# Performance work log

Hardware: AMD Instinct MI355X
Metric: run time of the kernel (lower is better)

Reference implementation:

```python
import jax, jax.numpy as jnp
import numpy as np

B, N, C = 8, 16384, 40
E, KD, VD = 512, 256, 256


def setup_inputs() -> dict:
    key = jax.random.key(0)
    ks = jax.random.split(key, 10)
    s = 0.02
    return {
        "q": jax.random.normal(ks[0], (B, N, E), jnp.float32),
        "k": jax.random.normal(ks[1], (B, C, KD), jnp.float32),
        "v": jax.random.normal(ks[2], (B, C, VD), jnp.float32),
        "coarse_pred": jax.random.normal(ks[3], (B, C, N), jnp.float32),
        "Wq": jax.random.normal(ks[4], (E, E), jnp.float32) * s,
        "bq": jnp.zeros((E,), jnp.float32),
        "Wk": jax.random.normal(ks[5], (E, KD), jnp.float32) * s,
        "bk": jnp.zeros((E,), jnp.float32),
        "Wv": jax.random.normal(ks[6], (E, VD), jnp.float32) * s,
        "bv": jnp.zeros((E,), jnp.float32),
    }


def reference(q, k, v, coarse_pred, Wq, bq, Wk, bk, Wv, bv):
    # Projections (nn.Linear: x @ W.T + b)
    qp = jnp.einsum("bne,fe->bnf", q, Wq) + bq          # (B, N, E)
    kp = jnp.einsum("bcd,fd->bcf", k, Wk) + bk          # (B, C, E)
    vp = jnp.einsum("bcd,fd->bcf", v, Wv) + bv          # (B, C, E)

    scale = 1.0 / jnp.sqrt(jnp.float32(E))
    attn = jnp.einsum("bne,bce->bnc", qp, kp) * scale   # (B, N, C)
    attn = jax.nn.softmax(attn, axis=-1)

    # coarse_pred is detached, transposed to (B, N, C), softmaxed over classes
    cp = jax.nn.softmax(jnp.swapaxes(coarse_pred, 1, 2), axis=-1)
    attn = jax.nn.softmax(attn * cp, axis=-1)

    out = jnp.einsum("bnc,bce->bne", attn, vp)          # (B, N, E)
    return out
```

## Files before the change

### kernel.cpp

```cpp
#include <hip/hip_runtime.h>
#include <hip/hip_bf16.h>
#include <stdint.h>

#define Bb 8
#define Nn 16384
#define Cc 40
#define Ee 512
#define Dd 256

typedef __attribute__((ext_vector_type(4))) float f32x4;
typedef __attribute__((ext_vector_type(8))) short bf16x8;

__device__ __forceinline__ unsigned short f2bf(float f) {
  union { float f; uint32_t u; } x; x.f = f;
  uint32_t r = x.u + 0x7FFFu + ((x.u >> 16) & 1u);
  return (unsigned short)(r >> 16);
}
__device__ __forceinline__ unsigned int pack2(float a, float b) {
  return (unsigned int)f2bf(a) | ((unsigned int)f2bf(b) << 16);
}
__device__ __forceinline__ bf16x8 q2bf(float4 a, float4 c) {
  union { __hip_bfloat162 h2[4]; bf16x8 v; } u;
  u.h2[0] = __float22bfloat162_rn(float2{a.x, a.y});
  u.h2[1] = __float22bfloat162_rn(float2{a.z, a.w});
  u.h2[2] = __float22bfloat162_rn(float2{c.x, c.y});
  u.h2[3] = __float22bfloat162_rn(float2{c.z, c.w});
  return u.v;
}

__global__ __launch_bounds__(256) void prepA_kernel(
    const float* __restrict__ Wq, const float* __restrict__ Wk,
    const float* __restrict__ bq, const float* __restrict__ bk,
    float* __restrict__ Mt, float* __restrict__ tvec,
    float* __restrict__ uvec, float* __restrict__ bqbk) {
  const int t = threadIdx.x;
  if (blockIdx.x == 8) {
    if (blockIdx.z != 0) return;
    const int by = blockIdx.y;
    if (by < 2) {
      const int e = by * 256 + t;
      float s = 0.f;
      #pragma unroll 8
      for (int f = 0; f < Ee; f++) s += Wq[(size_t)f * Ee + e] * bk[f];
      tvec[e] = s;
    } else if (by == 2) {
      const int d = t;
      float s = 0.f;
      #pragma unroll 8
      for (int f = 0; f < Ee; f++) s += Wk[(size_t)f * Dd + d] * bq[f];
      uvec[d] = s;
    } else {
      __shared__ float red[256];
      float p = 0.f;
      for (int f = t; f < Ee; f += 256) p += bq[f] * bk[f];
      red[t] = p; __syncthreads();
      #pragma unroll
      for (int off = 128; off > 0; off >>= 1) {
        if (t < off) red[t] += red[t + off];
        __syncthreads();
      }
      if (t == 0) bqbk[0] = red[0];
    }
    return;
  }
  __shared__ float WqL[64][68];
  __shared__ float WkL[64][68];
  const int te = (t & 15) * 4;
  const int td = (t >> 4) * 4;
  const int ebase = blockIdx.x * 64, dbase = blockIdx.y * 64;
  const int fbase = blockIdx.z * 256;
  f32x4 acc0 = {0,0,0,0}, acc1 = {0,0,0,0}, acc2 = {0,0,0,0}, acc3 = {0,0,0,0};
  for (int f0 = 0; f0 < 256; f0 += 64) {
    __syncthreads();
    #pragma unroll
    for (int i = 0; i < 4; i++) {
      int idx = t + i * 256;
      int row = idx >> 4, c4 = (idx & 15) * 4;
      *(float4*)&WqL[row][c4] = *(const float4*)(Wq + (size_t)(fbase + f0 + row) * Ee + ebase + c4);
      *(float4*)&WkL[row][c4] = *(const float4*)(Wk + (size_t)(fbase + f0 + row) * Dd + dbase + c4);
    }
    __syncthreads();
    #pragma unroll 8
    for (int ff = 0; ff < 64; ff++) {
      float4 a = *(const float4*)&WkL[ff][td];
      float4 b = *(const float4*)&WqL[ff][te];
      acc0[0] += a.x*b.x; acc0[1] += a.x*b.y; acc0[2] += a.x*b.z; acc0[3] += a.x*b.w;
      acc1[0] += a.y*b.x; acc1[1] += a.y*b.y; acc1[2] += a.y*b.z; acc1[3] += a.y*b.w;
      acc2[0] += a.z*b.x; acc2[1] += a.z*b.y; acc2[2] += a.z*b.z; acc2[3] += a.z*b.w;
      acc3[0] += a.w*b.x; acc3[1] += a.w*b.y; acc3[2] += a.w*b.z; acc3[3] += a.w*b.w;
    }
  }
  float* mt = Mt + (size_t)blockIdx.z * 131072;
  *(f32x4*)&mt[(size_t)(dbase + td + 0) * Ee + ebase + te] = acc0;
  *(f32x4*)&mt[(size_t)(dbase + td + 1) * Ee + ebase + te] = acc1;
  *(f32x4*)&mt[(size_t)(dbase + td + 2) * Ee + ebase + te] = acc2;
  *(f32x4*)&mt[(size_t)(dbase + td + 3) * Ee + ebase + te] = acc3;
}

__global__ __launch_bounds__(256) void prepB_kernel(
    const float* __restrict__ k, const float* __restrict__ v,
    const float* __restrict__ Wv, const float* __restrict__ bv,
    const float* __restrict__ Mt, const float* __restrict__ tvec,
    const float* __restrict__ uvec, const float* __restrict__ bqbk,
    unsigned short* __restrict__ abf, unsigned short* __restrict__ vpf,
    float* __restrict__ dbias) {
  __shared__ float xL[8][Dd];
  const int t = threadIdx.x;
  const int el = t & 127, half = t >> 7;
  const int e = blockIdx.y * 128 + el;

  if (blockIdx.x < 48) {
    const int sbase = blockIdx.x * 8;
    for (int i = t; i < 8 * Dd; i += 256) {
      int row = i >> 8, dd = i & (Dd - 1);
      int sg = sbase + row, bb_ = sg / 48, cc = sg % 48;
      xL[row][dd] = (cc < 40) ? k[((size_t)bb_ * Cc + cc) * Dd + dd] : 0.f;
    }
    __syncthreads();
    float acc[4] = {0,0,0,0};
    float db[4]  = {0,0,0,0};
    #pragma unroll 8
    for (int d = 0; d < Dd; d++) {
      float mt = Mt[(size_t)d * Ee + e] + Mt[131072 + (size_t)d * Ee + e];
      float ud = uvec[d];
      #pragma unroll
      for (int si = 0; si < 4; si++) {
        float kv = xL[half*4 + si][d];
        acc[si] += mt * kv;
        db[si]  += ud * kv;
      }
    }
    const float scale = 0.044194173824159216f;
    const float te = tvec[e];
    const float bqbkv = bqbk[0];
    const int ks = e >> 5, gg = (e >> 3) & 3, j = e & 7;
    #pragma unroll
    for (int si = 0; si < 4; si++) {
      int sg = sbase + half*4 + si, bb_ = sg / 48, cc = sg % 48;
      int ct = cc >> 4, lane16 = (cc & 15) + 16*gg;
      unsigned short val = (cc < 40) ? f2bf(scale * (acc[si] + te)) : (unsigned short)0;
      abf[((((size_t)bb_*3 + ct)*16 + ks)*64 + lane16)*8 + j] = val;
      if (el == 0) dbias[bb_*64 + cc] = (cc < 40) ? scale * (db[si] + bqbkv) : 0.f;
    }
  } else {
    const int sbase = (blockIdx.x - 48) * 8;
    for (int i = t; i < 8 * Dd; i += 256) {
      int row = i >> 8, dd = i & (Dd - 1);
      int sg = sbase + row, bb_ = sg >> 6, cc = sg & 63;
      xL[row][dd] = (cc < 40) ? v[((size_t)bb_ * Cc + cc) * Dd + dd] : 0.f;
    }
    __syncthreads();
    const float* wrow = Wv + (size_t)e * Dd;
    float acc[4] = {0,0,0,0};
    #pragma unroll 2
    for (int dd = 0; dd < Dd; dd += 4) {
      float4 w = *(const float4*)(wrow + dd);
      #pragma unroll
      for (int si = 0; si < 4; si++) {
        float4 vv = *(const float4*)&xL[half*4 + si][dd];
        acc[si] += w.x*vv.x + w.y*vv.y + w.z*vv.z + w.w*vv.w;
      }
    }
    const float bve = bv[e];
    const int nt = e >> 4, elan = e & 15;
    #pragma unroll
    for (int si = 0; si < 4; si++) {
      int sg = sbase + half*4 + si, bb_ = sg >> 6, cc = sg & 63;
      int s = cc >> 5, gg = (cc >> 3) & 3, j = cc & 7;
      unsigned short val = (cc < 40) ? f2bf(acc[si] + bve) : (unsigned short)0;
      vpf[((((size_t)bb_*32 + nt)*2 + s)*64 + (elan + 16*gg))*8 + j] = val;
    }
  }
}

__global__ __launch_bounds__(512, 2) void main_kernel(
    const float* __restrict__ q, const float* __restrict__ coarse,
    const unsigned short* __restrict__ abfrag,
    const unsigned short* __restrict__ vpfrag,
    const float* __restrict__ dbias, float* __restrict__ out) {
  __shared__ uint4 fragL[7168];
  __shared__ unsigned short s_att[8][16][72];
  const int t = threadIdx.x;
  const int wave = t >> 6, lane = t & 63;
  const int r = lane & 15, g = lane >> 4;
  const int b = blockIdx.x >> 5;
  const int seg = blockIdx.x & 31;
  const bool v2 = (g < 2);

  const float4 db0 = *(const float4*)(dbias + b*64 +  0 + 4*g);
  const float4 db1 = *(const float4*)(dbias + b*64 + 16 + 4*g);
  const float4 db2 = *(const float4*)(dbias + b*64 + 32 + 4*g);

  {
    const uint4* srcA = (const uint4*)abfrag + (size_t)b * 3072;
    #pragma unroll
    for (int i = 0; i < 6; i++) fragL[t + i*512] = srcA[t + i*512];
    const uint4* srcV = (const uint4*)vpfrag + (size_t)b * 4096;
    #pragma unroll
    for (int i = 0; i < 8; i++) fragL[3072 + t + i*512] = srcV[t + i*512];
  }
  __syncthreads();

  const int row0 = seg * 512 + wave * 16;
  const float* qrow0 = q + ((size_t)b * Nn + row0 + r) * Ee + 8 * g;
  const float* cbase0 = coarse + (size_t)b * Cc * Nn + row0 + r;
  float* outb0 = out + ((size_t)b * Nn + row0 + r) * Ee + 4 * g;

  f32x4 acc0, acc1, acc2;
  float4 H0[16], H1[16];

  auto LOADH = [&](const float* qr, int h, float4* H) {
    #pragma unroll
    for (int j = 0; j < 8; j++) {
      H[2*j]   = *(const float4*)(qr + 256*h + 32*j);
      H[2*j+1] = *(const float4*)(qr + 256*h + 32*j + 4);
    }
  };
  auto COMP = [&](const float4* H, int h) {
    #pragma unroll
    for (int j = 0; j < 8; j++) {
      bf16x8 qf = q2bf(H[2*j], H[2*j+1]);
      const int ks = 8*h + j;
      acc0 = __builtin_amdgcn_mfma_f32_16x16x32_bf16(*(const bf16x8*)&fragL[(0*16+ks)*64 + lane], qf, acc0, 0,0,0);
      acc1 = __builtin_amdgcn_mfma_f32_16x16x32_bf16(*(const bf16x8*)&fragL[(1*16+ks)*64 + lane], qf, acc1, 0,0,0);
      acc2 = __builtin_amdgcn_mfma_f32_16x16x32_bf16(*(const bf16x8*)&fragL[(2*16+ks)*64 + lane], qf, acc2, 0,0,0);
    }
  };

  LOADH(qrow0, 0, H0);

  for (int it = 0; it < 4; it++) {
    const float* qr = qrow0 + (size_t)(it*128) * Ee;
    LOADH(qr, 1, H1);
    acc0 = f32x4{0,0,0,0}; acc1 = f32x4{0,0,0,0}; acc2 = f32x4{0,0,0,0};
    COMP(H0, 0);

    const float* cb = cbase0 + it*128;
    float cr[3][4];
    #pragma unroll
    for (int rg = 0; rg < 4; rg++) {
      cr[0][rg] = cb[(size_t)( 0 + 4*g + rg) * Nn];
      cr[1][rg] = cb[(size_t)(16 + 4*g + rg) * Nn];
      cr[2][rg] = v2 ? cb[(size_t)(32 + 4*g + rg) * Nn] : -3e38f;
    }

    COMP(H1, 1);

    float L[3][4];
    #pragma unroll
    for (int rg = 0; rg < 4; rg++) {
      L[0][rg] = acc0[rg] + ((const float*)&db0)[rg];
      L[1][rg] = acc1[rg] + ((const float*)&db1)[rg];
      L[2][rg] = acc2[rg] + ((const float*)&db2)[rg];
    }

    float m1 = -3e38f;
    #pragma unroll
    for (int rg = 0; rg < 4; rg++) {
      m1 = fmaxf(m1, L[0][rg]); m1 = fmaxf(m1, L[1][rg]);
      if (v2) m1 = fmaxf(m1, L[2][rg]);
    }
    m1 = fmaxf(m1, __shfl_xor(m1, 16));
    m1 = fmaxf(m1, __shfl_xor(m1, 32));
    float p[3][4]; float s1 = 0.f;
    #pragma unroll
    for (int rg = 0; rg < 4; rg++) {
      p[0][rg] = __expf(L[0][rg] - m1); s1 += p[0][rg];
      p[1][rg] = __expf(L[1][rg] - m1); s1 += p[1][rg];
      p[2][rg] = v2 ? __expf(L[2][rg] - m1) : 0.f; s1 += p[2][rg];
    }
    s1 += __shfl_xor(s1, 16); s1 += __shfl_xor(s1, 32);
    const float inv1 = 1.0f / s1;

    float m2 = -3e38f;
    #pragma unroll
    for (int rg = 0; rg < 4; rg++) {
      m2 = fmaxf(m2, cr[0][rg]); m2 = fmaxf(m2, cr[1][rg]);
      if (v2) m2 = fmaxf(m2, cr[2][rg]);
    }
    m2 = fmaxf(m2, __shfl_xor(m2, 16));
    m2 = fmaxf(m2, __shfl_xor(m2, 32));
    float cpv[3][4]; float s2 = 0.f;
    #pragma unroll
    for (int rg = 0; rg < 4; rg++) {
      cpv[0][rg] = __expf(cr[0][rg] - m2); s2 += cpv[0][rg];
      cpv[1][rg] = __expf(cr[1][rg] - m2); s2 += cpv[1][rg];
      cpv[2][rg] = v2 ? __expf(cr[2][rg] - m2) : 0.f; s2 += cpv[2][rg];
    }
    s2 += __shfl_xor(s2, 16); s2 += __shfl_xor(s2, 32);
    const float inv2 = 1.0f / s2;

    const float sc12 = inv1 * inv2;
    float w[3][4];
    float m3 = -3e38f;
    #pragma unroll
    for (int rg = 0; rg < 4; rg++) {
      w[0][rg] = p[0][rg] * cpv[0][rg] * sc12;
      w[1][rg] = p[1][rg] * cpv[1][rg] * sc12;
      w[2][rg] = v2 ? (p[2][rg] * cpv[2][rg] * sc12) : 0.f;
      m3 = fmaxf(m3, w[0][rg]); m3 = fmaxf(m3, w[1][rg]);
      if (v2) m3 = fmaxf(m3, w[2][rg]);
    }
    m3 = fmaxf(m3, __shfl_xor(m3, 16));
    m3 = fmaxf(m3, __shfl_xor(m3, 32));
    float p3[3][4]; float s3 = 0.f;
    #pragma unroll
    for (int rg = 0; rg < 4; rg++) {
      p3[0][rg] = __expf(w[0][rg] - m3); s3 += p3[0][rg];
      p3[1][rg] = __expf(w[1][rg] - m3); s3 += p3[1][rg];
      p3[2][rg] = v2 ? __expf(w[2][rg] - m3) : 0.f; s3 += p3[2][rg];
    }
    s3 += __shfl_xor(s3, 16); s3 += __shfl_xor(s3, 32);
    const float inv3 = 1.0f / s3;

    if (it < 3) LOADH(qrow0 + (size_t)((it+1)*128) * Ee, 0, H0);

    unsigned int* srow = (unsigned int*)&s_att[wave][r][0];
    #pragma unroll
    for (int ct = 0; ct < 3; ct++) {
      srow[8*ct + 2*g + 0] = pack2(p3[ct][0]*inv3, p3[ct][1]*inv3);
      srow[8*ct + 2*g + 1] = pack2(p3[ct][2]*inv3, p3[ct][3]*inv3);
    }
    srow[24 + 2*g + 0] = 0u;
    srow[24 + 2*g + 1] = 0u;
    asm volatile("s_waitcnt lgkmcnt(0)" ::: "memory");
    const bf16x8 pa0 = *(const bf16x8*)&s_att[wave][r][ 0 + 8*g];
    const bf16x8 pa1 = *(const bf16x8*)&s_att[wave][r][32 + 8*g];

    float* outp = outb0 + (size_t)(it*128) * Ee;
    #pragma unroll 8
    for (int nt = 0; nt < 32; nt++) {
      bf16x8 vf0 = *(const bf16x8*)&fragL[3072 + (nt*2 + 0)*64 + lane];
      bf16x8 vf1 = *(const bf16x8*)&fragL[3072 + (nt*2 + 1)*64 + lane];
      f32x4 o = {0,0,0,0};
      o = __builtin_amdgcn_mfma_f32_16x16x32_bf16(vf0, pa0, o, 0,0,0);
      o = __builtin_amdgcn_mfma_f32_16x16x32_bf16(vf1, pa1, o, 0,0,0);
      *(f32x4*)(outp + nt*16) = o;
    }
  }
}

extern "C" void kernel_launch(void* const* d_in, const int* in_sizes, int n_in,
                              void* d_out, int out_size, void* d_ws, size_t ws_size,
                              hipStream_t stream) {
  const float* q   = (const float*)d_in[0];
  const float* k   = (const float*)d_in[1];
  const float* v   = (const float*)d_in[2];
  const float* cps = (const float*)d_in[3];
  const float* Wq  = (const float*)d_in[4];
  const float* bq  = (const float*)d_in[5];
  const float* Wk  = (const float*)d_in[6];
  const float* bk  = (const float*)d_in[7];
  const float* Wv  = (const float*)d_in[8];
  const float* bv  = (const float*)d_in[9];
  float* out = (float*)d_out;
  char* ws = (char*)d_ws;

  float*          Mt    = (float*)(ws);
  float*          tvec  = (float*)(ws + 1048576);
  float*          uvec  = (float*)(ws + 1050624);
  float*          bqbkp = (float*)(ws + 1051648);
  unsigned short* abf   = (unsigned short*)(ws + 1052672);
  unsigned short* vpf   = (unsigned short*)(ws + 1052672 + 393216);
  float*          dbias = (float*)(ws + 1052672 + 393216 + 524288);

  prepA_kernel<<<dim3(9, 4, 2), 256, 0, stream>>>(Wq, Wk, bq, bk, Mt, tvec, uvec, bqbkp);
  prepB_kernel<<<dim3(112, 4),  256, 0, stream>>>(k, v, Wv, bv, Mt, tvec, uvec, bqbkp,
                                                  abf, vpf, dbias);
  main_kernel <<<dim3(256),     512, 0, stream>>>(q, cps, abf, vpf, dbias, out);
}
```

Before: 174.6 us.

## Raise occupancy: stream V fragments from global, smaller Q register buffers, more blocks

After: 289.6 us. 1.66x slower.

```diff
diff --git a/kernel.cpp b/kernel.cpp
--- a/kernel.cpp
+++ b/kernel.cpp
@@ -173,18 +173,18 @@
   }
 }
 
-__global__ __launch_bounds__(512, 2) void main_kernel(
+__global__ __launch_bounds__(512, 4) void main_kernel(
     const float* __restrict__ q, const float* __restrict__ coarse,
     const unsigned short* __restrict__ abfrag,
     const unsigned short* __restrict__ vpfrag,
     const float* __restrict__ dbias, float* __restrict__ out) {
-  __shared__ uint4 fragL[7168];
+  __shared__ uint4 abL[3072];
   __shared__ unsigned short s_att[8][16][72];
   const int t = threadIdx.x;
   const int wave = t >> 6, lane = t & 63;
   const int r = lane & 15, g = lane >> 4;
-  const int b = blockIdx.x >> 5;
-  const int seg = blockIdx.x & 31;
+  const int b = blockIdx.x >> 6;
+  const int seg = blockIdx.x & 63;
   const bool v2 = (g < 2);
 
   const float4 db0 = *(const float4*)(dbias + b*64 +  0 + 4*g);
@@ -194,46 +194,42 @@
   {
     const uint4* srcA = (const uint4*)abfrag + (size_t)b * 3072;
     #pragma unroll
-    for (int i = 0; i < 6; i++) fragL[t + i*512] = srcA[t + i*512];
-    const uint4* srcV = (const uint4*)vpfrag + (size_t)b * 4096;
-    #pragma unroll
-    for (int i = 0; i < 8; i++) fragL[3072 + t + i*512] = srcV[t + i*512];
+    for (int i = 0; i < 6; i++) abL[t + i*512] = srcA[t + i*512];
   }
   __syncthreads();
 
-  const int row0 = seg * 512 + wave * 16;
+  const int row0 = seg * 256 + wave * 16;
   const float* qrow0 = q + ((size_t)b * Nn + row0 + r) * Ee + 8 * g;
   const float* cbase0 = coarse + (size_t)b * Cc * Nn + row0 + r;
   float* outb0 = out + ((size_t)b * Nn + row0 + r) * Ee + 4 * g;
+  const bf16x8* vpb = (const bf16x8*)vpfrag + (size_t)b * 4096 + lane;
 
   f32x4 acc0, acc1, acc2;
-  float4 H0[16], H1[16];
-
-  auto LOADH = [&](const float* qr, int h, float4* H) {
-    #pragma unroll
-    for (int j = 0; j < 8; j++) {
-      H[2*j]   = *(const float4*)(qr + 256*h + 32*j);
-      H[2*j+1] = *(const float4*)(qr + 256*h + 32*j + 4);
+  float4 QA[8], QB[8];
+
+  auto LOADQ = [&](const float* qr, int qi, float4* Q) {
+    #pragma unroll
+    for (int j = 0; j < 4; j++) {
+      Q[2*j]   = *(const float4*)(qr + 128*qi + 32*j);
+      Q[2*j+1] = *(const float4*)(qr + 128*qi + 32*j + 4);
     }
   };
-  auto COMP = [&](const float4* H, int h) {
-    #pragma unroll
-    for (int j = 0; j < 8; j++) {
-      bf16x8 qf = q2bf(H[2*j], H[2*j+1]);
-      const int ks = 8*h + j;
-      acc0 = __builtin_amdgcn_mfma_f32_16x16x32_bf16(*(const bf16x8*)&fragL[(0*16+ks)*64 + lane], qf, acc0, 0,0,0);
-      acc1 = __builtin_amdgcn_mfma_f32_16x16x32_bf16(*(const bf16x8*)&fragL[(1*16+ks)*64 + lane], qf, acc1, 0,0,0);
-      acc2 = __builtin_amdgcn_mfma_f32_16x16x32_bf16(*(const bf16x8*)&fragL[(2*16+ks)*64 + lane], qf, acc2, 0,0,0);
+  auto COMPQ = [&](const float4* Q, int qi) {
+    #pragma unroll
+    for (int j = 0; j < 4; j++) {
+      bf16x8 qf = q2bf(Q[2*j], Q[2*j+1]);
+      const int ks = 4*qi + j;
+      acc0 = __builtin_amdgcn_mfma_f32_16x16x32_bf16(*(const bf16x8*)&abL[(0*16+ks)*64 + lane], qf, acc0, 0,0,0);
+      acc1 = __builtin_amdgcn_mfma_f32_16x16x32_bf16(*(const bf16x8*)&abL[(1*16+ks)*64 + lane], qf, acc1, 0,0,0);
+      acc2 = __builtin_amdgcn_mfma_f32_16x16x32_bf16(*(const bf16x8*)&abL[(2*16+ks)*64 + lane], qf, acc2, 0,0,0);
     }
   };
 
-  LOADH(qrow0, 0, H0);
-
-  for (int it = 0; it < 4; it++) {
+  LOADQ(qrow0, 0, QA);
+
+  for (int it = 0; it < 2; it++) {
     const float* qr = qrow0 + (size_t)(it*128) * Ee;
-    LOADH(qr, 1, H1);
-    acc0 = f32x4{0,0,0,0}; acc1 = f32x4{0,0,0,0}; acc2 = f32x4{0,0,0,0};
-    COMP(H0, 0);
+    LOADQ(qr, 1, QB);
 
     const float* cb = cbase0 + it*128;
     float cr[3][4];
@@ -244,7 +240,11 @@
       cr[2][rg] = v2 ? cb[(size_t)(32 + 4*g + rg) * Nn] : -3e38f;
     }
 
-    COMP(H1, 1);
+    acc0 = f32x4{0,0,0,0}; acc1 = f32x4{0,0,0,0}; acc2 = f32x4{0,0,0,0};
+    COMPQ(QA, 0); LOADQ(qr, 2, QA);
+    COMPQ(QB, 1); LOADQ(qr, 3, QB);
+    COMPQ(QA, 2);
+    COMPQ(QB, 3);
 
     float L[3][4];
     #pragma unroll
@@ -313,7 +313,7 @@
     s3 += __shfl_xor(s3, 16); s3 += __shfl_xor(s3, 32);
     const float inv3 = 1.0f / s3;
 
-    if (it < 3) LOADH(qrow0 + (size_t)((it+1)*128) * Ee, 0, H0);
+    if (it < 1) LOADQ(qrow0 + (size_t)((it+1)*128) * Ee, 0, QA);
 
     unsigned int* srow = (unsigned int*)&s_att[wave][r][0];
     #pragma unroll
@@ -328,14 +328,16 @@
     const bf16x8 pa1 = *(const bf16x8*)&s_att[wave][r][32 + 8*g];
 
     float* outp = outb0 + (size_t)(it*128) * Ee;
-    #pragma unroll 8
+    bf16x8 va0 = vpb[0], va1 = vpb[64];
+    #pragma unroll
     for (int nt = 0; nt < 32; nt++) {
-      bf16x8 vf0 = *(const bf16x8*)&fragL[3072 + (nt*2 + 0)*64 + lane];
-      bf16x8 vf1 = *(const bf16x8*)&fragL[3072 + (nt*2 + 1)*64 + lane];
+      bf16x8 vb0, vb1;
+      if (nt < 31) { vb0 = vpb[(nt+1)*128]; vb1 = vpb[(nt+1)*128 + 64]; }
       f32x4 o = {0,0,0,0};
-      o = __builtin_amdgcn_mfma_f32_16x16x32_bf16(vf0, pa0, o, 0,0,0);
-      o = __builtin_amdgcn_mfma_f32_16x16x32_bf16(vf1, pa1, o, 0,0,0);
+      o = __builtin_amdgcn_mfma_f32_16x16x32_bf16(va0, pa0, o, 0,0,0);
+      o = __builtin_amdgcn_mfma_f32_16x16x32_bf16(va1, pa1, o, 0,0,0);
       *(f32x4*)(outp + nt*16) = o;
+      va0 = vb0; va1 = vb1;
     }
   }
 }
@@ -367,5 +369,5 @@
   prepA_kernel<<<dim3(9, 4, 2), 256, 0, stream>>>(Wq, Wk, bq, bk, Mt, tvec, uvec, bqbkp);
   prepB_kernel<<<dim3(112, 4),  256, 0, stream>>>(k, v, Wv, bv, Mt, tvec, uvec, bqbkp,
                                                   abf, vpf, dbias);
-  main_kernel <<<dim3(256),     512, 0, stream>>>(q, cps, abf, vpf, dbias, out);
-}
+  main_kernel <<<dim3(512),     512, 0, stream>>>(q, cps, abf, vpf, dbias, out);
+}
```

## Replace deep q prefetch with small double-buffered chunks to cut register pressure

Applied to the files above, without the earlier changes.

New measurement: 173.8 us. No clear change (-0.5%).

```diff
diff --git a/kernel.cpp b/kernel.cpp
--- a/kernel.cpp
+++ b/kernel.cpp
@@ -173,7 +173,7 @@
   }
 }
 
-__global__ __launch_bounds__(512, 2) void main_kernel(
+__global__ __launch_bounds__(512) void main_kernel(
     const float* __restrict__ q, const float* __restrict__ coarse,
     const unsigned short* __restrict__ abfrag,
     const unsigned short* __restrict__ vpfrag,
@@ -187,10 +187,6 @@
   const int seg = blockIdx.x & 31;
   const bool v2 = (g < 2);
 
-  const float4 db0 = *(const float4*)(dbias + b*64 +  0 + 4*g);
-  const float4 db1 = *(const float4*)(dbias + b*64 + 16 + 4*g);
-  const float4 db2 = *(const float4*)(dbias + b*64 + 32 + 4*g);
-
   {
     const uint4* srcA = (const uint4*)abfrag + (size_t)b * 3072;
     #pragma unroll
@@ -206,34 +202,36 @@
   const float* cbase0 = coarse + (size_t)b * Cc * Nn + row0 + r;
   float* outb0 = out + ((size_t)b * Nn + row0 + r) * Ee + 4 * g;
 
-  f32x4 acc0, acc1, acc2;
-  float4 H0[16], H1[16];
-
-  auto LOADH = [&](const float* qr, int h, float4* H) {
-    #pragma unroll
-    for (int j = 0; j < 8; j++) {
-      H[2*j]   = *(const float4*)(qr + 256*h + 32*j);
-      H[2*j+1] = *(const float4*)(qr + 256*h + 32*j + 4);
-    }
-  };
-  auto COMP = [&](const float4* H, int h) {
-    #pragma unroll
-    for (int j = 0; j < 8; j++) {
-      bf16x8 qf = q2bf(H[2*j], H[2*j+1]);
-      const int ks = 8*h + j;
-      acc0 = __builtin_amdgcn_mfma_f32_16x16x32_bf16(*(const bf16x8*)&fragL[(0*16+ks)*64 + lane], qf, acc0, 0,0,0);
-      acc1 = __builtin_amdgcn_mfma_f32_16x16x32_bf16(*(const bf16x8*)&fragL[(1*16+ks)*64 + lane], qf, acc1, 0,0,0);
-      acc2 = __builtin_amdgcn_mfma_f32_16x16x32_bf16(*(const bf16x8*)&fragL[(2*16+ks)*64 + lane], qf, acc2, 0,0,0);
-    }
-  };
-
-  LOADH(qrow0, 0, H0);
-
   for (int it = 0; it < 4; it++) {
     const float* qr = qrow0 + (size_t)(it*128) * Ee;
-    LOADH(qr, 1, H1);
-    acc0 = f32x4{0,0,0,0}; acc1 = f32x4{0,0,0,0}; acc2 = f32x4{0,0,0,0};
-    COMP(H0, 0);
+    f32x4 acc0 = {0,0,0,0}, acc1 = {0,0,0,0}, acc2 = {0,0,0,0};
+
+    float4 a0, a1, a2, a3, b0, b1, b2, b3;
+    auto LD_A = [&](int c) {
+      a0 = *(const float4*)(qr + 64*c);
+      a1 = *(const float4*)(qr + 64*c + 4);
+      a2 = *(const float4*)(qr + 64*c + 32);
+      a3 = *(const float4*)(qr + 64*c + 36);
+    };
+    auto LD_B = [&](int c) {
+      b0 = *(const float4*)(qr + 64*c);
+      b1 = *(const float4*)(qr + 64*c + 4);
+      b2 = *(const float4*)(qr + 64*c + 32);
+      b3 = *(const float4*)(qr + 64*c + 36);
+    };
+    auto MM = [&](int c, float4 x0, float4 x1, float4 x2, float4 x3) {
+      bf16x8 q0 = q2bf(x0, x1), q1 = q2bf(x2, x3);
+      const int ks = 2*c;
+      acc0 = __builtin_amdgcn_mfma_f32_16x16x32_bf16(*(const bf16x8*)&fragL[(0*16+ks)*64 + lane], q0, acc0, 0,0,0);
+      acc1 = __builtin_amdgcn_mfma_f32_16x16x32_bf16(*(const bf16x8*)&fragL[(1*16+ks)*64 + lane], q0, acc1, 0,0,0);
+      acc2 = __builtin_amdgcn_mfma_f32_16x16x32_bf16(*(const bf16x8*)&fragL[(2*16+ks)*64 + lane], q0, acc2, 0,0,0);
+      acc0 = __builtin_amdgcn_mfma_f32_16x16x32_bf16(*(const bf16x8*)&fragL[(0*16+ks+1)*64 + lane], q1, acc0, 0,0,0);
+      acc1 = __builtin_amdgcn_mfma_f32_16x16x32_bf16(*(const bf16x8*)&fragL[(1*16+ks+1)*64 + lane], q1, acc1, 0,0,0);
+      acc2 = __builtin_amdgcn_mfma_f32_16x16x32_bf16(*(const bf16x8*)&fragL[(2*16+ks+1)*64 + lane], q1, acc2, 0,0,0);
+    };
+
+    LD_A(0);
+    LD_B(1);
 
     const float* cb = cbase0 + it*128;
     float cr[3][4];
@@ -244,33 +242,43 @@
       cr[2][rg] = v2 ? cb[(size_t)(32 + 4*g + rg) * Nn] : -3e38f;
     }
 
-    COMP(H1, 1);
-
-    float L[3][4];
-    #pragma unroll
-    for (int rg = 0; rg < 4; rg++) {
-      L[0][rg] = acc0[rg] + ((const float*)&db0)[rg];
-      L[1][rg] = acc1[rg] + ((const float*)&db1)[rg];
-      L[2][rg] = acc2[rg] + ((const float*)&db2)[rg];
+    MM(0, a0,a1,a2,a3); LD_A(2);
+    MM(1, b0,b1,b2,b3); LD_B(3);
+    MM(2, a0,a1,a2,a3); LD_A(4);
+    MM(3, b0,b1,b2,b3); LD_B(5);
+    MM(4, a0,a1,a2,a3); LD_A(6);
+    MM(5, b0,b1,b2,b3); LD_B(7);
+    MM(6, a0,a1,a2,a3);
+    MM(7, b0,b1,b2,b3);
+
+    const float4 db0 = *(const float4*)(dbias + b*64 +  0 + 4*g);
+    const float4 db1 = *(const float4*)(dbias + b*64 + 16 + 4*g);
+    const float4 db2 = *(const float4*)(dbias + b*64 + 32 + 4*g);
+
+    float x[3][4];
+    #pragma unroll
+    for (int rg = 0; rg < 4; rg++) {
+      x[0][rg] = acc0[rg] + ((const float*)&db0)[rg];
+      x[1][rg] = acc1[rg] + ((const float*)&db1)[rg];
+      x[2][rg] = acc2[rg] + ((const float*)&db2)[rg];
     }
 
     float m1 = -3e38f;
     #pragma unroll
     for (int rg = 0; rg < 4; rg++) {
-      m1 = fmaxf(m1, L[0][rg]); m1 = fmaxf(m1, L[1][rg]);
-      if (v2) m1 = fmaxf(m1, L[2][rg]);
+      m1 = fmaxf(m1, x[0][rg]); m1 = fmaxf(m1, x[1][rg]);
+      if (v2) m1 = fmaxf(m1, x[2][rg]);
     }
     m1 = fmaxf(m1, __shfl_xor(m1, 16));
     m1 = fmaxf(m1, __shfl_xor(m1, 32));
-    float p[3][4]; float s1 = 0.f;
-    #pragma unroll
-    for (int rg = 0; rg < 4; rg++) {
-      p[0][rg] = __expf(L[0][rg] - m1); s1 += p[0][rg];
-      p[1][rg] = __expf(L[1][rg] - m1); s1 += p[1][rg];
-      p[2][rg] = v2 ? __expf(L[2][rg] - m1) : 0.f; s1 += p[2][rg];
+    float s1 = 0.f;
+    #pragma unroll
+    for (int rg = 0; rg < 4; rg++) {
+      x[0][rg] = __expf(x[0][rg] - m1); s1 += x[0][rg];
+      x[1][rg] = __expf(x[1][rg] - m1); s1 += x[1][rg];
+      x[2][rg] = v2 ? __expf(x[2][rg] - m1) : 0.f; s1 += x[2][rg];
     }
     s1 += __shfl_xor(s1, 16); s1 += __shfl_xor(s1, 32);
-    const float inv1 = 1.0f / s1;
 
     float m2 = -3e38f;
     #pragma unroll
@@ -280,46 +288,42 @@
     }
     m2 = fmaxf(m2, __shfl_xor(m2, 16));
     m2 = fmaxf(m2, __shfl_xor(m2, 32));
-    float cpv[3][4]; float s2 = 0.f;
-    #pragma unroll
-    for (int rg = 0; rg < 4; rg++) {
-      cpv[0][rg] = __expf(cr[0][rg] - m2); s2 += cpv[0][rg];
-      cpv[1][rg] = __expf(cr[1][rg] - m2); s2 += cpv[1][rg];
-      cpv[2][rg] = v2 ? __expf(cr[2][rg] - m2) : 0.f; s2 += cpv[2][rg];
+    float s2 = 0.f;
+    #pragma unroll
+    for (int rg = 0; rg < 4; rg++) {
+      cr[0][rg] = __expf(cr[0][rg] - m2); s2 += cr[0][rg];
+      cr[1][rg] = __expf(cr[1][rg] - m2); s2 += cr[1][rg];
+      cr[2][rg] = v2 ? __expf(cr[2][rg] - m2) : 0.f; s2 += cr[2][rg];
     }
     s2 += __shfl_xor(s2, 16); s2 += __shfl_xor(s2, 32);
-    const float inv2 = 1.0f / s2;
-
-    const float sc12 = inv1 * inv2;
-    float w[3][4];
+
+    const float sc12 = 1.0f / (s1 * s2);
     float m3 = -3e38f;
     #pragma unroll
     for (int rg = 0; rg < 4; rg++) {
-      w[0][rg] = p[0][rg] * cpv[0][rg] * sc12;
-      w[1][rg] = p[1][rg] * cpv[1][rg] * sc12;
-      w[2][rg] = v2 ? (p[2][rg] * cpv[2][rg] * sc12) : 0.f;
-      m3 = fmaxf(m3, w[0][rg]); m3 = fmaxf(m3, w[1][rg]);
-      if (v2) m3 = fmaxf(m3, w[2][rg]);
+      x[0][rg] *= cr[0][rg] * sc12;
+      x[1][rg] *= cr[1][rg] * sc12;
+      x[2][rg] = v2 ? (x[2][rg] * cr[2][rg] * sc12) : 0.f;
+      m3 = fmaxf(m3, x[0][rg]); m3 = fmaxf(m3, x[1][rg]);
+      if (v2) m3 = fmaxf(m3, x[2][rg]);
     }
     m3 = fmaxf(m3, __shfl_xor(m3, 16));
     m3 = fmaxf(m3, __shfl_xor(m3, 32));
-    float p3[3][4]; float s3 = 0.f;
-    #pragma unroll
-    for (int rg = 0; rg < 4; rg++) {
-      p3[0][rg] = __expf(w[0][rg] - m3); s3 += p3[0][rg];
-      p3[1][rg] = __expf(w[1][rg] - m3); s3 += p3[1][rg];
-      p3[2][rg] = v2 ? __expf(w[2][rg] - m3) : 0.f; s3 += p3[2][rg];
+    float s3 = 0.f;
+    #pragma unroll
+    for (int rg = 0; rg < 4; rg++) {
+      x[0][rg] = __expf(x[0][rg] - m3); s3 += x[0][rg];
+      x[1][rg] = __expf(x[1][rg] - m3); s3 += x[1][rg];
+      x[2][rg] = v2 ? __expf(x[2][rg] - m3) : 0.f; s3 += x[2][rg];
     }
     s3 += __shfl_xor(s3, 16); s3 += __shfl_xor(s3, 32);
     const float inv3 = 1.0f / s3;
 
-    if (it < 3) LOADH(qrow0 + (size_t)((it+1)*128) * Ee, 0, H0);
-
     unsigned int* srow = (unsigned int*)&s_att[wave][r][0];
     #pragma unroll
     for (int ct = 0; ct < 3; ct++) {
-      srow[8*ct + 2*g + 0] = pack2(p3[ct][0]*inv3, p3[ct][1]*inv3);
-      srow[8*ct + 2*g + 1] = pack2(p3[ct][2]*inv3, p3[ct][3]*inv3);
+      srow[8*ct + 2*g + 0] = pack2(x[ct][0]*inv3, x[ct][1]*inv3);
+      srow[8*ct + 2*g + 1] = pack2(x[ct][2]*inv3, x[ct][3]*inv3);
     }
     srow[24 + 2*g + 0] = 0u;
     srow[24 + 2*g + 1] = 0u;
```
